# Performance work log

Measured on AMD Instinct MI355X. Metric: run time of the kernel, lower is better.

Reference implementation:

```python
import jax, jax.numpy as jnp
import numpy as np

N = 10000      # num nodes
E = 320000     # num edges
IN = 256       # in_dim
MP = 256       # mp_width
FL = 512       # fl_width
OUT = 64       # out_dim


def setup_inputs() -> dict:
    key = jax.random.key(0)
    ks = jax.random.split(key, 20)
    inp = {}
    inp["x"] = jax.random.normal(ks[0], (N, IN), dtype=jnp.float32)
    inp["edge_index"] = jax.random.randint(ks[1], (2, E), 0, N, dtype=jnp.int64)
    # iMP (frozen) linear layers: weight ~ N(0, 1) per nn.init.normal_(std=1.0)
    inp["mp_w0"] = jax.random.normal(ks[2], (IN, MP), dtype=jnp.float32)
    inp["mp_b0"] = jax.random.uniform(ks[3], (MP,), minval=-1.0, maxval=1.0) / np.sqrt(IN)
    inp["mp_w1"] = jax.random.normal(ks[4], (MP, MP), dtype=jnp.float32)
    inp["mp_b1"] = jax.random.uniform(ks[5], (MP,), minval=-1.0, maxval=1.0) / np.sqrt(MP)
    inp["mp_w2"] = jax.random.normal(ks[6], (MP, MP), dtype=jnp.float32)
    inp["mp_b2"] = jax.random.uniform(ks[7], (MP,), minval=-1.0, maxval=1.0) / np.sqrt(MP)
    # FC layers (torch default Linear init scale ~ 1/sqrt(fan_in))
    inp["fc_w0"] = jax.random.normal(ks[8], (MP, FL), dtype=jnp.float32) / np.sqrt(MP)
    inp["fc_b0"] = jnp.zeros((FL,), dtype=jnp.float32)
    inp["fc_w1"] = jax.random.normal(ks[9], (FL, FL), dtype=jnp.float32) / np.sqrt(FL)
    inp["fc_b1"] = jnp.zeros((FL,), dtype=jnp.float32)
    # injection projections
    inp["inj_w0"] = jax.random.normal(ks[10], (MP, FL), dtype=jnp.float32) / np.sqrt(MP)
    inp["inj_b0"] = jnp.zeros((FL,), dtype=jnp.float32)
    inp["inj_w1"] = jax.random.normal(ks[11], (MP, FL), dtype=jnp.float32) / np.sqrt(MP)
    inp["inj_b1"] = jnp.zeros((FL,), dtype=jnp.float32)
    inp["alpha"] = jnp.array(1.0, dtype=jnp.float32)
    inp["out_w"] = jax.random.normal(ks[12], (FL, OUT), dtype=jnp.float32) / np.sqrt(FL)
    inp["out_b"] = jnp.zeros((OUT,), dtype=jnp.float32)
    return inp


def _imp(x, w, b, row, col, deg_inv):
    # h = relu(W x); h /= deg; Ah = scatter_add over row of h[col]
    h = jax.nn.relu(x @ w + b) * deg_inv[:, None]      # [N, out]
    return jnp.zeros_like(h).at[row].add(h[col])       # gather + scatter-add


def reference(x, edge_index, mp_w0, mp_b0, mp_w1, mp_b1, mp_w2, mp_b2,
              fc_w0, fc_b0, fc_w1, fc_b1, inj_w0, inj_b0, inj_w1, inj_b1,
              alpha, out_w, out_b):
    row, col = edge_index[0], edge_index[1]
    deg = jax.ops.segment_sum(jnp.ones((E,), x.dtype), col, num_segments=N)
    # nodes with deg==0 never appear in col so clamping does not change output
    deg_inv = 1.0 / jnp.maximum(deg, 1.0)

    h = _imp(x, mp_w0, mp_b0, row, col, deg_inv)
    h = _imp(h, mp_w1, mp_b1, row, col, deg_inv)
    h = _imp(h, mp_w2, mp_b2, row, col, deg_inv)

    x_inject = h
    h = alpha * (jax.nn.relu(h) @ fc_w0 + fc_b0) + (x_inject @ inj_w0 + inj_b0)
    h = alpha * (jax.nn.relu(h) @ fc_w1 + fc_b1) + (x_inject @ inj_w1 + inj_b1)
    return h @ out_w + out_b
```

## Files before the change

### kernel.cpp

```cpp
#include <hip/hip_runtime.h>

#define N_NODES 10000
#define N_EDGES 320000
#define MPAD 10112
#define NBIN 10048
#define CAP 128
#define EBLKS 157
#define PREP_BLOCKS 768
#define PREP_TOT 656384L

typedef unsigned short u16;
typedef short bf16x8 __attribute__((ext_vector_type(8)));
typedef float f32x4 __attribute__((ext_vector_type(4)));

__device__ __forceinline__ u16 f2b(float f) {
  unsigned u = __builtin_bit_cast(unsigned, f);
  unsigned r = u + 0x7fffu + ((u >> 16) & 1u);
  return (u16)(r >> 16);
}
__device__ __forceinline__ unsigned pack2(float a, float b) {
  return (unsigned)f2b(a) | ((unsigned)f2b(b) << 16);
}
__device__ __forceinline__ float blo(unsigned u) { return __builtin_bit_cast(float, u << 16); }
__device__ __forceinline__ float bhi(unsigned u) { return __builtin_bit_cast(float, u & 0xffff0000u); }
__device__ __forceinline__ int4 cvt16(float4 a, float4 b) {
  int4 r;
  r.x = (int)pack2(a.x, a.y); r.y = (int)pack2(a.z, a.w);
  r.z = (int)pack2(b.x, b.y); r.w = (int)pack2(b.z, b.w);
  return r;
}

struct PP {
  const float *x; const int *ei;
  const float *w0, *w1, *w2, *fcw0, *injw0, *fcw1, *injw1, *outw;
  const float *fcb0, *injb0, *fcb1, *injb1, *alpha, *outb;
  u16 *w0t, *w1t, *w2t, *wc1t, *wft;
  float *bias1, *bf;
  int *cursor, *deg; u16 *csr;
};

__global__ __launch_bounds__(256) void prep_place(PP P) {
  const int tid = threadIdx.x, bid = blockIdx.x;

  if (bid < EBLKS) {
    const int e0 = bid * 2048;
#pragma unroll
    for (int j = 0; j < 2048; j += 256) {
      int e = e0 + j + tid;
      if (e < N_EDGES) {
        int r = P.ei[e];
        int c = P.ei[N_EDGES + e];
        atomicAdd(&P.deg[c], 1);
        int pos = atomicAdd(&P.cursor[r], 1);
        if (pos < CAP) P.csr[r * CAP + pos] = (u16)c;
      }
    }
    return;
  }

  const float alpha = P.alpha[0];
  const long stride = (long)PREP_BLOCKS * 256;
  for (long ii = (long)(bid - EBLKS) * 256 + tid; ii < PREP_TOT; ii += stride) {
    long i = ii;
    if (i < 196608) {
      int item = (int)(i >> 2), part = (int)i & 3;
      int n = item & 63, k = item >> 6;
      const float* fr = (k < 512) ? P.fcw1 + (size_t)k * 512
                                  : P.injw1 + (size_t)(k - 512) * 512;
      float a0 = 0.f, a1 = 0.f, a2 = 0.f, a3 = 0.f;
      const int j0 = part * 128;
#pragma unroll 4
      for (int j = j0; j < j0 + 128; j += 4) {
        float4 f = *(const float4*)(fr + j);
        a0 += f.x * P.outw[(j + 0) * 64 + n];
        a1 += f.y * P.outw[(j + 1) * 64 + n];
        a2 += f.z * P.outw[(j + 2) * 64 + n];
        a3 += f.w * P.outw[(j + 3) * 64 + n];
      }
      float acc = (a0 + a1) + (a2 + a3);
      acc += __shfl_xor(acc, 1, 64);
      acc += __shfl_xor(acc, 2, 64);
      if (part == 0) {
        if (k < 512) acc *= alpha;
        P.wft[n * 768 + k] = f2b(acc);
      }
      continue;
    }
    i -= 196608;
    if (i < 512) {
      int item = (int)(i >> 3), part = (int)i & 7;
      float acc = 0.f;
      const int j0 = part * 64;
#pragma unroll 4
      for (int j = j0; j < j0 + 64; ++j)
        acc += (alpha * P.fcb1[j] + P.injb1[j]) * P.outw[j * 64 + item];
      acc += __shfl_xor(acc, 1, 64);
      acc += __shfl_xor(acc, 2, 64);
      acc += __shfl_xor(acc, 4, 64);
      if (part == 0) P.bf[item] = P.outb[item] + acc;
      continue;
    }
    i -= 512;
    if (i < 65536) { P.w0t[i] = f2b(P.w0[(i & 255) * 256 + (i >> 8)]); continue; }
    i -= 65536;
    if (i < 65536) { P.w1t[i] = f2b(P.w1[(i & 255) * 256 + (i >> 8)]); continue; }
    i -= 65536;
    if (i < 65536) { P.w2t[i] = f2b(P.w2[(i & 255) * 256 + (i >> 8)]); continue; }
    i -= 65536;
    if (i < 262144) {
      int n = (int)(i >> 9), k = (int)(i & 511);
      float v = (k < 256) ? alpha * P.fcw0[k * 512 + n] : P.injw0[(k - 256) * 512 + n];
      P.wc1t[i] = f2b(v); continue;
    }
    i -= 262144;
    if (i < 512) { P.bias1[i] = alpha * P.fcb0[i] + P.injb0[i]; continue; }
  }
}

template<int K, bool RELU, bool SCALE, bool F32OUT, bool AF32>
__global__ __launch_bounds__(128) void gemm64(
    const void* __restrict__ Av, int lda,
    const u16* __restrict__ Bt,
    const float* __restrict__ bias,
    const int* __restrict__ deg,
    u16* __restrict__ Cb, float* __restrict__ Cf, int ldc)
{
  __shared__ u16 As[64 * 72];
  __shared__ u16 Bs[64 * 72];
  const int tid = threadIdx.x;
  const int m0 = blockIdx.x * 64;
  const int n0 = blockIdx.y * 64;
  const int wave = tid >> 6;
  const int lane = tid & 63;
  const int wr = wave * 32;
  const int lm = lane & 15;
  const int koff = (lane >> 4) * 8;

  const int srow = tid >> 2;
  const int scol = (tid & 3) * 16;
  const u16 *Ag0 = nullptr, *Ag1 = nullptr;
  const float *Af0 = nullptr, *Af1 = nullptr;
  if constexpr (AF32) {
    const int ar0 = min(m0 + srow, N_NODES - 1);
    const int ar1 = min(m0 + srow + 32, N_NODES - 1);
    Af0 = (const float*)Av + (size_t)ar0 * lda + scol;
    Af1 = (const float*)Av + (size_t)ar1 * lda + scol;
  } else {
    Ag0 = (const u16*)Av + (size_t)(m0 + srow) * lda + scol;
    Ag1 = (const u16*)Av + (size_t)(m0 + srow + 32) * lda + scol;
  }
  const u16* Bg0 = Bt + (size_t)(n0 + srow) * K + scol;
  const u16* Bg1 = Bt + (size_t)(n0 + srow + 32) * K + scol;
  u16* Asw0 = &As[srow * 72 + scol];
  u16* Asw1 = &As[(srow + 32) * 72 + scol];
  u16* Bsw0 = &Bs[srow * 72 + scol];
  u16* Bsw1 = &Bs[(srow + 32) * 72 + scol];

  f32x4 acc[2][4] = {};

  int4 pa0, pa1, pa2, pa3;
  if constexpr (AF32) {
    float4 f0 = *(const float4*)(Af0),     f1 = *(const float4*)(Af0 + 4);
    float4 f2 = *(const float4*)(Af0 + 8), f3 = *(const float4*)(Af0 + 12);
    float4 g0 = *(const float4*)(Af1),     g1 = *(const float4*)(Af1 + 4);
    float4 g2 = *(const float4*)(Af1 + 8), g3 = *(const float4*)(Af1 + 12);
    pa0 = cvt16(f0, f1); pa1 = cvt16(f2, f3);
    pa2 = cvt16(g0, g1); pa3 = cvt16(g2, g3);
  } else {
    pa0 = *(const int4*)(Ag0); pa1 = *(const int4*)(Ag0 + 8);
    pa2 = *(const int4*)(Ag1); pa3 = *(const int4*)(Ag1 + 8);
  }
  int4 pb0 = *(const int4*)(Bg0),     pb1 = *(const int4*)(Bg0 + 8);
  int4 pb2 = *(const int4*)(Bg1),     pb3 = *(const int4*)(Bg1 + 8);

#pragma unroll
  for (int kb = 0; kb < K; kb += 64) {
    __syncthreads();
    *(int4*)Asw0 = pa0; *(int4*)(Asw0 + 8) = pa1;
    *(int4*)Asw1 = pa2; *(int4*)(Asw1 + 8) = pa3;
    *(int4*)Bsw0 = pb0; *(int4*)(Bsw0 + 8) = pb1;
    *(int4*)Bsw1 = pb2; *(int4*)(Bsw1 + 8) = pb3;
    __syncthreads();
    if (kb + 64 < K) {
      if constexpr (AF32) {
        const float* a0 = Af0 + kb + 64;
        const float* a1 = Af1 + kb + 64;
        float4 f0 = *(const float4*)(a0),     f1 = *(const float4*)(a0 + 4);
        float4 f2 = *(const float4*)(a0 + 8), f3 = *(const float4*)(a0 + 12);
        float4 g0 = *(const float4*)(a1),     g1 = *(const float4*)(a1 + 4);
        float4 g2 = *(const float4*)(a1 + 8), g3 = *(const float4*)(a1 + 12);
        pa0 = cvt16(f0, f1); pa1 = cvt16(f2, f3);
        pa2 = cvt16(g0, g1); pa3 = cvt16(g2, g3);
      } else {
        pa0 = *(const int4*)(Ag0 + kb + 64); pa1 = *(const int4*)(Ag0 + kb + 72);
        pa2 = *(const int4*)(Ag1 + kb + 64); pa3 = *(const int4*)(Ag1 + kb + 72);
      }
      pb0 = *(const int4*)(Bg0 + kb + 64); pb1 = *(const int4*)(Bg0 + kb + 72);
      pb2 = *(const int4*)(Bg1 + kb + 64); pb3 = *(const int4*)(Bg1 + kb + 72);
    }
#pragma unroll
    for (int ks = 0; ks < 2; ++ks) {
      bf16x8 af[2], bf[4];
#pragma unroll
      for (int mi = 0; mi < 2; ++mi)
        af[mi] = *(const bf16x8*)&As[(wr + mi * 16 + lm) * 72 + ks * 32 + koff];
#pragma unroll
      for (int ni = 0; ni < 4; ++ni)
        bf[ni] = *(const bf16x8*)&Bs[(ni * 16 + lm) * 72 + ks * 32 + koff];
#pragma unroll
      for (int mi = 0; mi < 2; ++mi)
#pragma unroll
        for (int ni = 0; ni < 4; ++ni)
          acc[mi][ni] = __builtin_amdgcn_mfma_f32_16x16x32_bf16(af[mi], bf[ni], acc[mi][ni], 0, 0, 0);
    }
  }

  const int q4 = (lane >> 4) * 4;
#pragma unroll
  for (int mi = 0; mi < 2; ++mi) {
#pragma unroll
    for (int ni = 0; ni < 4; ++ni) {
      const int gc = n0 + ni * 16 + lm;
      const float bv = bias[gc];
#pragma unroll
      for (int r = 0; r < 4; ++r) {
        const int gr = m0 + wr + mi * 16 + q4 + r;
        float v = acc[mi][ni][r] + bv;
        if (RELU) v = fmaxf(v, 0.f);
        if (SCALE) v *= 1.0f / fmaxf((float)deg[gr], 1.0f);
        if (F32OUT) {
          if (gr < N_NODES) Cf[(size_t)gr * ldc + gc] = v;
        } else {
          Cb[(size_t)gr * ldc + gc] = f2b(v);
        }
      }
    }
  }
}

__global__ __launch_bounds__(128) void gemm_fold(
    const u16* __restrict__ Ar,
    const u16* __restrict__ Ah,
    const u16* __restrict__ Bt,
    const float* __restrict__ bias,
    float* __restrict__ Cf)
{
  const int K = 768;
  __shared__ u16 As[64 * 72];
  __shared__ u16 Bs[64 * 72];
  const int tid = threadIdx.x;
  const int m0 = blockIdx.x * 64;
  const int n0 = 0;
  const int wave = tid >> 6;
  const int lane = tid & 63;
  const int wr = wave * 32;
  const int lm = lane & 15;
  const int koff = (lane >> 4) * 8;

  const int srow = tid >> 2;
  const int scol = (tid & 3) * 16;
  const int ar0 = m0 + srow, ar1 = m0 + srow + 32;
  auto aptr = [&](int row, int col) -> const u16* {
    return (col < 512) ? Ar + (size_t)row * 512 + col
                       : Ah + (size_t)row * 512 + (col - 512);
  };
  const u16* Bg0 = Bt + (size_t)(n0 + srow) * K + scol;
  const u16* Bg1 = Bt + (size_t)(n0 + srow + 32) * K + scol;
  u16* Asw0 = &As[srow * 72 + scol];
  u16* Asw1 = &As[(srow + 32) * 72 + scol];
  u16* Bsw0 = &Bs[srow * 72 + scol];
  u16* Bsw1 = &Bs[(srow + 32) * 72 + scol];

  f32x4 acc[2][4] = {};

  int4 pa0 = *(const int4*)aptr(ar0, scol);
  int4 pa1 = *(const int4*)aptr(ar0, scol + 8);
  int4 pa2 = *(const int4*)aptr(ar1, scol);
  int4 pa3 = *(const int4*)aptr(ar1, scol + 8);
  int4 pb0 = *(const int4*)(Bg0), pb1 = *(const int4*)(Bg0 + 8);
  int4 pb2 = *(const int4*)(Bg1), pb3 = *(const int4*)(Bg1 + 8);

#pragma unroll
  for (int kb = 0; kb < K; kb += 64) {
    __syncthreads();
    *(int4*)Asw0 = pa0; *(int4*)(Asw0 + 8) = pa1;
    *(int4*)Asw1 = pa2; *(int4*)(Asw1 + 8) = pa3;
    *(int4*)Bsw0 = pb0; *(int4*)(Bsw0 + 8) = pb1;
    *(int4*)Bsw1 = pb2; *(int4*)(Bsw1 + 8) = pb3;
    __syncthreads();
    if (kb + 64 < K) {
      int c = kb + 64 + scol;
      pa0 = *(const int4*)aptr(ar0, c);
      pa1 = *(const int4*)aptr(ar0, c + 8);
      pa2 = *(const int4*)aptr(ar1, c);
      pa3 = *(const int4*)aptr(ar1, c + 8);
      pb0 = *(const int4*)(Bg0 + kb + 64); pb1 = *(const int4*)(Bg0 + kb + 72);
      pb2 = *(const int4*)(Bg1 + kb + 64); pb3 = *(const int4*)(Bg1 + kb + 72);
    }
#pragma unroll
    for (int ks = 0; ks < 2; ++ks) {
      bf16x8 af[2], bf[4];
#pragma unroll
      for (int mi = 0; mi < 2; ++mi)
        af[mi] = *(const bf16x8*)&As[(wr + mi * 16 + lm) * 72 + ks * 32 + koff];
#pragma unroll
      for (int ni = 0; ni < 4; ++ni)
        bf[ni] = *(const bf16x8*)&Bs[(ni * 16 + lm) * 72 + ks * 32 + koff];
#pragma unroll
      for (int mi = 0; mi < 2; ++mi)
#pragma unroll
        for (int ni = 0; ni < 4; ++ni)
          acc[mi][ni] = __builtin_amdgcn_mfma_f32_16x16x32_bf16(af[mi], bf[ni], acc[mi][ni], 0, 0, 0);
    }
  }

  const int q4 = (lane >> 4) * 4;
#pragma unroll
  for (int mi = 0; mi < 2; ++mi) {
#pragma unroll
    for (int ni = 0; ni < 4; ++ni) {
      const int gc = ni * 16 + lm;
      const float bv = bias[gc];
#pragma unroll
      for (int r = 0; r < 4; ++r) {
        const int gr = m0 + wr + mi * 16 + q4 + r;
        if (gr < N_NODES) Cf[(size_t)gr * 64 + gc] = acc[mi][ni][r] + bv;
      }
    }
  }
}

__global__ __launch_bounds__(256) void aggregate(
    const u16* __restrict__ tmp, const int* __restrict__ cnt,
    const u16* __restrict__ csr, u16* __restrict__ out0,
    u16* __restrict__ A1, int mode)
{
  const int wv = threadIdx.x >> 6;
  const int lane = threadIdx.x & 63;
  const int r = blockIdx.x * 4 + wv;
  const int half = lane >> 5;
  const int q = lane & 31;
  int n = cnt[r]; if (n > CAP) n = CAP;
  const int beg = r * CAP, end = beg + n;
  const size_t feat = (size_t)q * 16;
  const char* tb = (const char*)tmp;

  float s0 = 0.f, s1 = 0.f, s2 = 0.f, s3 = 0.f, s4 = 0.f, s5 = 0.f, s6 = 0.f, s7 = 0.f;
  int i = beg;
  for (; i + 8 <= end; i += 8) {
    uint4 v[4];
#pragma unroll
    for (int j = 0; j < 4; ++j)
      v[j] = *(const uint4*)(tb + (size_t)csr[i + 2 * j + half] * 512 + feat);
#pragma unroll
    for (int j = 0; j < 4; ++j) {
      s0 += blo(v[j].x); s1 += bhi(v[j].x); s2 += blo(v[j].y); s3 += bhi(v[j].y);
      s4 += blo(v[j].z); s5 += bhi(v[j].z); s6 += blo(v[j].w); s7 += bhi(v[j].w);
    }
  }
  for (; i < end; i += 2) {
    int id = i + half;
    if (id < end) {
      uint4 v = *(const uint4*)(tb + (size_t)csr[id] * 512 + feat);
      s0 += blo(v.x); s1 += bhi(v.x); s2 += blo(v.y); s3 += bhi(v.y);
      s4 += blo(v.z); s5 += bhi(v.z); s6 += blo(v.w); s7 += bhi(v.w);
    }
  }
  const int src = lane ^ 32;
  s0 += __shfl(s0, src, 64); s1 += __shfl(s1, src, 64);
  s2 += __shfl(s2, src, 64); s3 += __shfl(s3, src, 64);
  s4 += __shfl(s4, src, 64); s5 += __shfl(s5, src, 64);
  s6 += __shfl(s6, src, 64); s7 += __shfl(s7, src, 64);

  if (half == 0) {
    uint4 pv;
    pv.x = pack2(s0, s1); pv.y = pack2(s2, s3);
    pv.z = pack2(s4, s5); pv.w = pack2(s6, s7);
    if (mode == 0) {
      *(uint4*)((char*)out0 + (size_t)r * 512 + feat) = pv;
    } else {
      uint4 pr;
      pr.x = pack2(fmaxf(s0, 0.f), fmaxf(s1, 0.f));
      pr.y = pack2(fmaxf(s2, 0.f), fmaxf(s3, 0.f));
      pr.z = pack2(fmaxf(s4, 0.f), fmaxf(s5, 0.f));
      pr.w = pack2(fmaxf(s6, 0.f), fmaxf(s7, 0.f));
      *(uint4*)((char*)A1 + (size_t)r * 1024 + feat) = pr;
      *(uint4*)((char*)A1 + (size_t)r * 1024 + 512 + feat) = pv;
    }
  }
}

extern "C" void kernel_launch(void* const* d_in, const int* in_sizes, int n_in,
                              void* d_out, int out_size, void* d_ws, size_t ws_size,
                              hipStream_t stream) {
  const int* ei = (const int*)d_in[1];

  char* p = (char*)d_ws;
  auto carve = [&](size_t bytes) -> void* {
    void* r = (void*)p;
    p += (bytes + 255) & ~(size_t)255;
    return r;
  };
  int*   deg     = (int*)carve(MPAD * 4);
  int*   cursor  = (int*)carve(NBIN * 4);
  u16*   csr     = (u16*)carve((size_t)NBIN * CAP * 2);
  float* bias1   = (float*)carve(512 * 4);
  float* bf      = (float*)carve(64 * 4);
  u16* w0t   = (u16*)carve(65536 * 2);
  u16* w1t   = (u16*)carve(65536 * 2);
  u16* w2t   = (u16*)carve(65536 * 2);
  u16* wc1t  = (u16*)carve(262144 * 2);
  u16* wft   = (u16*)carve(49152 * 2);
  u16* tmp   = (u16*)carve((size_t)MPAD * 256 * 2);
  u16* h     = (u16*)carve((size_t)MPAD * 256 * 2);
  u16* cat1  = (u16*)carve((size_t)MPAD * 512 * 2);
  u16* relu1 = (u16*)carve((size_t)MPAD * 512 * 2);

  PP pp;
  pp.x = (const float*)d_in[0];
  pp.ei = ei;
  pp.w0 = (const float*)d_in[2];
  pp.w1 = (const float*)d_in[4];
  pp.w2 = (const float*)d_in[6];
  pp.fcw0 = (const float*)d_in[8];
  pp.fcw1 = (const float*)d_in[10];
  pp.injw0 = (const float*)d_in[12];
  pp.injw1 = (const float*)d_in[14];
  pp.outw = (const float*)d_in[17];
  pp.fcb0 = (const float*)d_in[9];
  pp.injb0 = (const float*)d_in[13];
  pp.fcb1 = (const float*)d_in[11];
  pp.injb1 = (const float*)d_in[15];
  pp.alpha = (const float*)d_in[16];
  pp.outb = (const float*)d_in[18];
  pp.w0t = w0t; pp.w1t = w1t; pp.w2t = w2t;
  pp.wc1t = wc1t; pp.wft = wft;
  pp.bias1 = bias1; pp.bf = bf;
  pp.cursor = cursor; pp.deg = deg; pp.csr = csr;

  const float* mp_b0 = (const float*)d_in[3];
  const float* mp_b1 = (const float*)d_in[5];
  const float* mp_b2 = (const float*)d_in[7];
  float* out = (float*)d_out;

  hipMemsetAsync(deg, 0, (size_t)(MPAD + NBIN) * 4, stream);
  prep_place<<<EBLKS + PREP_BLOCKS, 256, 0, stream>>>(pp);

  dim3 gmp(MPAD / 64, 4), gfc(MPAD / 64, 8), go(MPAD / 64, 1);
  gemm64<256, true, true, false, true ><<<gmp, 128, 0, stream>>>(pp.x, 256, w0t, mp_b0, deg, tmp, nullptr, 256);
  aggregate<<<2500, 256, 0, stream>>>(tmp, cursor, csr, h, nullptr, 0);
  gemm64<256, true, true, false, false><<<gmp, 128, 0, stream>>>(h, 256, w1t, mp_b1, deg, tmp, nullptr, 256);
  aggregate<<<2500, 256, 0, stream>>>(tmp, cursor, csr, h, nullptr, 0);
  gemm64<256, true, true, false, false><<<gmp, 128, 0, stream>>>(h, 256, w2t, mp_b2, deg, tmp, nullptr, 256);
  aggregate<<<2500, 256, 0, stream>>>(tmp, cursor, csr, nullptr, cat1, 1);
  gemm64<512, true, false, false, false><<<gfc, 128, 0, stream>>>(cat1, 512, wc1t, bias1, nullptr, relu1, nullptr, 512);
  gemm_fold<<<go, 128, 0, stream>>>(relu1, cat1 + 256, wft, bf, out);
}
```

Baseline: 245.3 us.

## Fuse first MP GEMM into prep kernel and split aggregation into feature halves

```diff
diff --git a/kernel.cpp b/kernel.cpp
--- a/kernel.cpp
+++ b/kernel.cpp
@@ -5,9 +5,13 @@
 #define MPAD 10112
 #define NBIN 10048
 #define CAP 128
-#define EBLKS 157
-#define PREP_BLOCKS 768
-#define PREP_TOT 656384L
+
+#define E1BLKS 313
+#define G1BLKS 632
+#define WB0    (E1BLKS + G1BLKS)
+#define WBLKS  1536
+#define GRID1  (WB0 + WBLKS)
+#define WPREP_TOT 590848L
 
 typedef unsigned short u16;
 typedef short bf16x8 __attribute__((ext_vector_type(8)));
@@ -29,60 +33,144 @@
   r.z = (int)pack2(b.x, b.y); r.w = (int)pack2(b.z, b.w);
   return r;
 }
+__device__ __forceinline__ void ldA(const float* a, int4& lo, int4& hi) {
+  float4 f0 = *(const float4*)(a),     f1 = *(const float4*)(a + 4);
+  float4 f2 = *(const float4*)(a + 8), f3 = *(const float4*)(a + 12);
+  lo = cvt16(f0, f1); hi = cvt16(f2, f3);
+}
+__device__ __forceinline__ void ldB(const float* w, int n, int k0, int4& lo, int4& hi) {
+  const float* p = w + (size_t)k0 * 256 + n;
+  lo.x = (int)pack2(p[0],    p[256]);  lo.y = (int)pack2(p[512],  p[768]);
+  lo.z = (int)pack2(p[1024], p[1280]); lo.w = (int)pack2(p[1536], p[1792]);
+  hi.x = (int)pack2(p[2048], p[2304]); hi.y = (int)pack2(p[2560], p[2816]);
+  hi.z = (int)pack2(p[3072], p[3328]); hi.w = (int)pack2(p[3584], p[3840]);
+}
 
 struct PP {
   const float *x; const int *ei;
   const float *w0, *w1, *w2, *fcw0, *injw0, *fcw1, *injw1, *outw;
-  const float *fcb0, *injb0, *fcb1, *injb1, *alpha, *outb;
-  u16 *w0t, *w1t, *w2t, *wc1t, *wft;
+  const float *fcb0, *injb0, *fcb1, *injb1, *alpha, *outb, *b0;
+  u16 *w1t, *w2t, *wc1t, *wft, *tmp;
   float *bias1, *bf;
   int *cursor, *deg; u16 *csr;
 };
 
-__global__ __launch_bounds__(256) void prep_place(PP P) {
+__global__ __launch_bounds__(128, 4) void fused1(PP F) {
   const int tid = threadIdx.x, bid = blockIdx.x;
-
-  if (bid < EBLKS) {
-    const int e0 = bid * 2048;
-#pragma unroll
-    for (int j = 0; j < 2048; j += 256) {
+  __shared__ u16 As[64 * 72];
+  __shared__ u16 Bs[64 * 72];
+
+  if (bid < E1BLKS) {
+    const int e0 = bid * 1024;
+#pragma unroll
+    for (int j = 0; j < 1024; j += 128) {
       int e = e0 + j + tid;
       if (e < N_EDGES) {
-        int r = P.ei[e];
-        int c = P.ei[N_EDGES + e];
-        atomicAdd(&P.deg[c], 1);
-        int pos = atomicAdd(&P.cursor[r], 1);
-        if (pos < CAP) P.csr[r * CAP + pos] = (u16)c;
+        int r = F.ei[e];
+        int c = F.ei[N_EDGES + e];
+        atomicAdd(&F.deg[c], 1);
+        int pos = atomicAdd(&F.cursor[r], 1);
+        if (pos < CAP) F.csr[r * CAP + pos] = (u16)c;
       }
     }
     return;
   }
 
-  const float alpha = P.alpha[0];
-  const long stride = (long)PREP_BLOCKS * 256;
-  for (long ii = (long)(bid - EBLKS) * 256 + tid; ii < PREP_TOT; ii += stride) {
+  if (bid < WB0) {
+    const int gb = bid - E1BLKS;
+    const int m0 = (gb >> 2) * 64;
+    const int n0 = (gb & 3) * 64;
+    const int wave = tid >> 6, lane = tid & 63;
+    const int wr = wave * 32, lm = lane & 15, koff = (lane >> 4) * 8;
+    const int srow = tid >> 2, scol = (tid & 3) * 16;
+
+    const int ar0 = min(m0 + srow, N_NODES - 1);
+    const int ar1 = min(m0 + srow + 32, N_NODES - 1);
+    const float* Af0 = F.x + (size_t)ar0 * 256 + scol;
+    const float* Af1 = F.x + (size_t)ar1 * 256 + scol;
+    const int bn0 = n0 + srow, bn1 = n0 + srow + 32;
+    u16* Asw0 = &As[srow * 72 + scol];
+    u16* Asw1 = &As[(srow + 32) * 72 + scol];
+    u16* Bsw0 = &Bs[srow * 72 + scol];
+    u16* Bsw1 = &Bs[(srow + 32) * 72 + scol];
+
+    f32x4 acc[2][4] = {};
+    int4 pa0, pa1, pa2, pa3, pb0, pb1, pb2, pb3;
+    ldA(Af0, pa0, pa1); ldA(Af1, pa2, pa3);
+    ldB(F.w0, bn0, scol, pb0, pb1); ldB(F.w0, bn1, scol, pb2, pb3);
+
+#pragma unroll
+    for (int kb = 0; kb < 256; kb += 64) {
+      __syncthreads();
+      *(int4*)Asw0 = pa0; *(int4*)(Asw0 + 8) = pa1;
+      *(int4*)Asw1 = pa2; *(int4*)(Asw1 + 8) = pa3;
+      *(int4*)Bsw0 = pb0; *(int4*)(Bsw0 + 8) = pb1;
+      *(int4*)Bsw1 = pb2; *(int4*)(Bsw1 + 8) = pb3;
+      __syncthreads();
+      if (kb + 64 < 256) {
+        ldA(Af0 + kb + 64, pa0, pa1); ldA(Af1 + kb + 64, pa2, pa3);
+        ldB(F.w0, bn0, kb + 64 + scol, pb0, pb1);
+        ldB(F.w0, bn1, kb + 64 + scol, pb2, pb3);
+      }
+#pragma unroll
+      for (int ks = 0; ks < 2; ++ks) {
+        bf16x8 af[2], bfr[4];
+#pragma unroll
+        for (int mi = 0; mi < 2; ++mi)
+          af[mi] = *(const bf16x8*)&As[(wr + mi * 16 + lm) * 72 + ks * 32 + koff];
+#pragma unroll
+        for (int ni = 0; ni < 4; ++ni)
+          bfr[ni] = *(const bf16x8*)&Bs[(ni * 16 + lm) * 72 + ks * 32 + koff];
+#pragma unroll
+        for (int mi = 0; mi < 2; ++mi)
+#pragma unroll
+          for (int ni = 0; ni < 4; ++ni)
+            acc[mi][ni] = __builtin_amdgcn_mfma_f32_16x16x32_bf16(af[mi], bfr[ni], acc[mi][ni], 0, 0, 0);
+      }
+    }
+
+    const int q4 = (lane >> 4) * 4;
+#pragma unroll
+    for (int mi = 0; mi < 2; ++mi) {
+#pragma unroll
+      for (int ni = 0; ni < 4; ++ni) {
+        const int gc = n0 + ni * 16 + lm;
+        const float bv = F.b0[gc];
+#pragma unroll
+        for (int r = 0; r < 4; ++r) {
+          const int gr = m0 + wr + mi * 16 + q4 + r;
+          F.tmp[(size_t)gr * 256 + gc] = f2b(fmaxf(acc[mi][ni][r] + bv, 0.f));
+        }
+      }
+    }
+    return;
+  }
+
+  const float alpha = F.alpha[0];
+  const long stride = (long)WBLKS * 128;
+  for (long ii = (long)(bid - WB0) * 128 + tid; ii < WPREP_TOT; ii += stride) {
     long i = ii;
     if (i < 196608) {
       int item = (int)(i >> 2), part = (int)i & 3;
       int n = item & 63, k = item >> 6;
-      const float* fr = (k < 512) ? P.fcw1 + (size_t)k * 512
-                                  : P.injw1 + (size_t)(k - 512) * 512;
+      const float* fr = (k < 512) ? F.fcw1 + (size_t)k * 512
+                                  : F.injw1 + (size_t)(k - 512) * 512;
       float a0 = 0.f, a1 = 0.f, a2 = 0.f, a3 = 0.f;
       const int j0 = part * 128;
 #pragma unroll 4
       for (int j = j0; j < j0 + 128; j += 4) {
         float4 f = *(const float4*)(fr + j);
-        a0 += f.x * P.outw[(j + 0) * 64 + n];
-        a1 += f.y * P.outw[(j + 1) * 64 + n];
-        a2 += f.z * P.outw[(j + 2) * 64 + n];
-        a3 += f.w * P.outw[(j + 3) * 64 + n];
+        a0 += f.x * F.outw[(j + 0) * 64 + n];
+        a1 += f.y * F.outw[(j + 1) * 64 + n];
+        a2 += f.z * F.outw[(j + 2) * 64 + n];
+        a3 += f.w * F.outw[(j + 3) * 64 + n];
       }
       float acc = (a0 + a1) + (a2 + a3);
       acc += __shfl_xor(acc, 1, 64);
       acc += __shfl_xor(acc, 2, 64);
       if (part == 0) {
         if (k < 512) acc *= alpha;
-        P.wft[n * 768 + k] = f2b(acc);
+        F.wft[n * 768 + k] = f2b(acc);
       }
       continue;
     }
@@ -93,33 +181,31 @@
       const int j0 = part * 64;
 #pragma unroll 4
       for (int j = j0; j < j0 + 64; ++j)
-        acc += (alpha * P.fcb1[j] + P.injb1[j]) * P.outw[j * 64 + item];
+        acc += (alpha * F.fcb1[j] + F.injb1[j]) * F.outw[j * 64 + item];
       acc += __shfl_xor(acc, 1, 64);
       acc += __shfl_xor(acc, 2, 64);
       acc += __shfl_xor(acc, 4, 64);
-      if (part == 0) P.bf[item] = P.outb[item] + acc;
+      if (part == 0) F.bf[item] = F.outb[item] + acc;
       continue;
     }
     i -= 512;
-    if (i < 65536) { P.w0t[i] = f2b(P.w0[(i & 255) * 256 + (i >> 8)]); continue; }
+    if (i < 65536) { F.w1t[i] = f2b(F.w1[(i & 255) * 256 + (i >> 8)]); continue; }
     i -= 65536;
-    if (i < 65536) { P.w1t[i] = f2b(P.w1[(i & 255) * 256 + (i >> 8)]); continue; }
-    i -= 65536;
-    if (i < 65536) { P.w2t[i] = f2b(P.w2[(i & 255) * 256 + (i >> 8)]); continue; }
+    if (i < 65536) { F.w2t[i] = f2b(F.w2[(i & 255) * 256 + (i >> 8)]); continue; }
     i -= 65536;
     if (i < 262144) {
       int n = (int)(i >> 9), k = (int)(i & 511);
-      float v = (k < 256) ? alpha * P.fcw0[k * 512 + n] : P.injw0[(k - 256) * 512 + n];
-      P.wc1t[i] = f2b(v); continue;
+      float v = (k < 256) ? alpha * F.fcw0[k * 512 + n] : F.injw0[(k - 256) * 512 + n];
+      F.wc1t[i] = f2b(v); continue;
     }
     i -= 262144;
-    if (i < 512) { P.bias1[i] = alpha * P.fcb0[i] + P.injb0[i]; continue; }
-  }
-}
-
-template<int K, bool RELU, bool SCALE, bool F32OUT, bool AF32>
+    if (i < 512) { F.bias1[i] = alpha * F.fcb0[i] + F.injb0[i]; continue; }
+  }
+}
+
+template<int K, bool RELU, bool SCALE, bool F32OUT>
 __global__ __launch_bounds__(128) void gemm64(
-    const void* __restrict__ Av, int lda,
+    const u16* __restrict__ A, int lda,
     const u16* __restrict__ Bt,
     const float* __restrict__ bias,
     const int* __restrict__ deg,
@@ -138,17 +224,8 @@
 
   const int srow = tid >> 2;
   const int scol = (tid & 3) * 16;
-  const u16 *Ag0 = nullptr, *Ag1 = nullptr;
-  const float *Af0 = nullptr, *Af1 = nullptr;
-  if constexpr (AF32) {
-    const int ar0 = min(m0 + srow, N_NODES - 1);
-    const int ar1 = min(m0 + srow + 32, N_NODES - 1);
-    Af0 = (const float*)Av + (size_t)ar0 * lda + scol;
-    Af1 = (const float*)Av + (size_t)ar1 * lda + scol;
-  } else {
-    Ag0 = (const u16*)Av + (size_t)(m0 + srow) * lda + scol;
-    Ag1 = (const u16*)Av + (size_t)(m0 + srow + 32) * lda + scol;
-  }
+  const u16* Ag0 = A + (size_t)(m0 + srow) * lda + scol;
+  const u16* Ag1 = A + (size_t)(m0 + srow + 32) * lda + scol;
   const u16* Bg0 = Bt + (size_t)(n0 + srow) * K + scol;
   const u16* Bg1 = Bt + (size_t)(n0 + srow + 32) * K + scol;
   u16* Asw0 = &As[srow * 72 + scol];
@@ -158,18 +235,8 @@
 
   f32x4 acc[2][4] = {};
 
-  int4 pa0, pa1, pa2, pa3;
-  if constexpr (AF32) {
-    float4 f0 = *(const float4*)(Af0),     f1 = *(const float4*)(Af0 + 4);
-    float4 f2 = *(const float4*)(Af0 + 8), f3 = *(const float4*)(Af0 + 12);
-    float4 g0 = *(const float4*)(Af1),     g1 = *(const float4*)(Af1 + 4);
-    float4 g2 = *(const float4*)(Af1 + 8), g3 = *(const float4*)(Af1 + 12);
-    pa0 = cvt16(f0, f1); pa1 = cvt16(f2, f3);
-    pa2 = cvt16(g0, g1); pa3 = cvt16(g2, g3);
-  } else {
-    pa0 = *(const int4*)(Ag0); pa1 = *(const int4*)(Ag0 + 8);
-    pa2 = *(const int4*)(Ag1); pa3 = *(const int4*)(Ag1 + 8);
-  }
+  int4 pa0 = *(const int4*)(Ag0),     pa1 = *(const int4*)(Ag0 + 8);
+  int4 pa2 = *(const int4*)(Ag1),     pa3 = *(const int4*)(Ag1 + 8);
   int4 pb0 = *(const int4*)(Bg0),     pb1 = *(const int4*)(Bg0 + 8);
   int4 pb2 = *(const int4*)(Bg1),     pb3 = *(const int4*)(Bg1 + 8);
 
@@ -182,19 +249,8 @@
     *(int4*)Bsw1 = pb2; *(int4*)(Bsw1 + 8) = pb3;
     __syncthreads();
     if (kb + 64 < K) {
-      if constexpr (AF32) {
-        const float* a0 = Af0 + kb + 64;
-        const float* a1 = Af1 + kb + 64;
-        float4 f0 = *(const float4*)(a0),     f1 = *(const float4*)(a0 + 4);
-        float4 f2 = *(const float4*)(a0 + 8), f3 = *(const float4*)(a0 + 12);
-        float4 g0 = *(const float4*)(a1),     g1 = *(const float4*)(a1 + 4);
-        float4 g2 = *(const float4*)(a1 + 8), g3 = *(const float4*)(a1 + 12);
-        pa0 = cvt16(f0, f1); pa1 = cvt16(f2, f3);
-        pa2 = cvt16(g0, g1); pa3 = cvt16(g2, g3);
-      } else {
-        pa0 = *(const int4*)(Ag0 + kb + 64); pa1 = *(const int4*)(Ag0 + kb + 72);
-        pa2 = *(const int4*)(Ag1 + kb + 64); pa3 = *(const int4*)(Ag1 + kb + 72);
-      }
+      pa0 = *(const int4*)(Ag0 + kb + 64); pa1 = *(const int4*)(Ag0 + kb + 72);
+      pa2 = *(const int4*)(Ag1 + kb + 64); pa3 = *(const int4*)(Ag1 + kb + 72);
       pb0 = *(const int4*)(Bg0 + kb + 64); pb1 = *(const int4*)(Bg0 + kb + 72);
       pb2 = *(const int4*)(Bg1 + kb + 64); pb3 = *(const int4*)(Bg1 + kb + 72);
     }
@@ -330,10 +386,11 @@
   }
 }
 
+template<bool DSC>
 __global__ __launch_bounds__(256) void aggregate(
     const u16* __restrict__ tmp, const int* __restrict__ cnt,
-    const u16* __restrict__ csr, u16* __restrict__ out0,
-    u16* __restrict__ A1, int mode)
+    const u16* __restrict__ csr, const int* __restrict__ deg,
+    u16* __restrict__ out0, u16* __restrict__ A1, int mode, int fh)
 {
   const int wv = threadIdx.x >> 6;
   const int lane = threadIdx.x & 63;
@@ -342,50 +399,55 @@
   const int q = lane & 31;
   int n = cnt[r]; if (n > CAP) n = CAP;
   const int beg = r * CAP, end = beg + n;
-  const size_t feat = (size_t)q * 16;
+  const size_t feat = (size_t)fh * 256 + (size_t)q * 8;
   const char* tb = (const char*)tmp;
 
-  float s0 = 0.f, s1 = 0.f, s2 = 0.f, s3 = 0.f, s4 = 0.f, s5 = 0.f, s6 = 0.f, s7 = 0.f;
+  float s0 = 0.f, s1 = 0.f, s2 = 0.f, s3 = 0.f;
   int i = beg;
   for (; i + 8 <= end; i += 8) {
-    uint4 v[4];
-#pragma unroll
-    for (int j = 0; j < 4; ++j)
-      v[j] = *(const uint4*)(tb + (size_t)csr[i + 2 * j + half] * 512 + feat);
+    uint2 v[4]; float sc[4];
 #pragma unroll
     for (int j = 0; j < 4; ++j) {
-      s0 += blo(v[j].x); s1 += bhi(v[j].x); s2 += blo(v[j].y); s3 += bhi(v[j].y);
-      s4 += blo(v[j].z); s5 += bhi(v[j].z); s6 += blo(v[j].w); s7 += bhi(v[j].w);
+      int c = csr[i + 2 * j + half];
+      v[j] = *(const uint2*)(tb + (size_t)c * 512 + feat);
+      sc[j] = DSC ? 1.0f / fmaxf((float)deg[c], 1.0f) : 1.0f;
+    }
+#pragma unroll
+    for (int j = 0; j < 4; ++j) {
+      if (DSC) {
+        s0 += sc[j] * blo(v[j].x); s1 += sc[j] * bhi(v[j].x);
+        s2 += sc[j] * blo(v[j].y); s3 += sc[j] * bhi(v[j].y);
+      } else {
+        s0 += blo(v[j].x); s1 += bhi(v[j].x);
+        s2 += blo(v[j].y); s3 += bhi(v[j].y);
+      }
     }
   }
   for (; i < end; i += 2) {
     int id = i + half;
     if (id < end) {
-      uint4 v = *(const uint4*)(tb + (size_t)csr[id] * 512 + feat);
-      s0 += blo(v.x); s1 += bhi(v.x); s2 += blo(v.y); s3 += bhi(v.y);
-      s4 += blo(v.z); s5 += bhi(v.z); s6 += blo(v.w); s7 += bhi(v.w);
+      int c = csr[id];
+      uint2 v = *(const uint2*)(tb + (size_t)c * 512 + feat);
+      float sc = DSC ? 1.0f / fmaxf((float)deg[c], 1.0f) : 1.0f;
+      s0 += sc * blo(v.x); s1 += sc * bhi(v.x);
+      s2 += sc * blo(v.y); s3 += sc * bhi(v.y);
     }
   }
   const int src = lane ^ 32;
   s0 += __shfl(s0, src, 64); s1 += __shfl(s1, src, 64);
   s2 += __shfl(s2, src, 64); s3 += __shfl(s3, src, 64);
-  s4 += __shfl(s4, src, 64); s5 += __shfl(s5, src, 64);
-  s6 += __shfl(s6, src, 64); s7 += __shfl(s7, src, 64);
 
   if (half == 0) {
-    uint4 pv;
+    uint2 pv;
     pv.x = pack2(s0, s1); pv.y = pack2(s2, s3);
-    pv.z = pack2(s4, s5); pv.w = pack2(s6, s7);
     if (mode == 0) {
-      *(uint4*)((char*)out0 + (size_t)r * 512 + feat) = pv;
+      *(uint2*)((char*)out0 + (size_t)r * 512 + feat) = pv;
     } else {
-      uint4 pr;
+      uint2 pr;
       pr.x = pack2(fmaxf(s0, 0.f), fmaxf(s1, 0.f));
       pr.y = pack2(fmaxf(s2, 0.f), fmaxf(s3, 0.f));
-      pr.z = pack2(fmaxf(s4, 0.f), fmaxf(s5, 0.f));
-      pr.w = pack2(fmaxf(s6, 0.f), fmaxf(s7, 0.f));
-      *(uint4*)((char*)A1 + (size_t)r * 1024 + feat) = pr;
-      *(uint4*)((char*)A1 + (size_t)r * 1024 + 512 + feat) = pv;
+      *(uint2*)((char*)A1 + (size_t)r * 1024 + feat) = pr;
+      *(uint2*)((char*)A1 + (size_t)r * 1024 + 512 + feat) = pv;
     }
   }
 }
@@ -406,7 +468,6 @@
   u16*   csr     = (u16*)carve((size_t)NBIN * CAP * 2);
   float* bias1   = (float*)carve(512 * 4);
   float* bf      = (float*)carve(64 * 4);
-  u16* w0t   = (u16*)carve(65536 * 2);
   u16* w1t   = (u16*)carve(65536 * 2);
   u16* w2t   = (u16*)carve(65536 * 2);
   u16* wc1t  = (u16*)carve(262144 * 2);
@@ -433,26 +494,28 @@
   pp.injb1 = (const float*)d_in[15];
   pp.alpha = (const float*)d_in[16];
   pp.outb = (const float*)d_in[18];
-  pp.w0t = w0t; pp.w1t = w1t; pp.w2t = w2t;
-  pp.wc1t = wc1t; pp.wft = wft;
+  pp.b0 = (const float*)d_in[3];
+  pp.w1t = w1t; pp.w2t = w2t;
+  pp.wc1t = wc1t; pp.wft = wft; pp.tmp = tmp;
   pp.bias1 = bias1; pp.bf = bf;
   pp.cursor = cursor; pp.deg = deg; pp.csr = csr;
 
-  const float* mp_b0 = (const float*)d_in[3];
   const float* mp_b1 = (const float*)d_in[5];
   const float* mp_b2 = (const float*)d_in[7];
   float* out = (float*)d_out;
 
   hipMemsetAsync(deg, 0, (size_t)(MPAD + NBIN) * 4, stream);
-  prep_place<<<EBLKS + PREP_BLOCKS, 256, 0, stream>>>(pp);
+  fused1<<<GRID1, 128, 0, stream>>>(pp);
 
   dim3 gmp(MPAD / 64, 4), gfc(MPAD / 64, 8), go(MPAD / 64, 1);
-  gemm64<256, true, true, false, true ><<<gmp, 128, 0, stream>>>(pp.x, 256, w0t, mp_b0, deg, tmp, nullptr, 256);
-  aggregate<<<2500, 256, 0, stream>>>(tmp, cursor, csr, h, nullptr, 0);
-  gemm64<256, true, true, false, false><<<gmp, 128, 0, stream>>>(h, 256, w1t, mp_b1, deg, tmp, nullptr, 256);
-  aggregate<<<2500, 256, 0, stream>>>(tmp, cursor, csr, h, nullptr, 0);
-  gemm64<256, true, true, false, false><<<gmp, 128, 0, stream>>>(h, 256, w2t, mp_b2, deg, tmp, nullptr, 256);
-  aggregate<<<2500, 256, 0, stream>>>(tmp, cursor, csr, nullptr, cat1, 1);
-  gemm64<512, true, false, false, false><<<gfc, 128, 0, stream>>>(cat1, 512, wc1t, bias1, nullptr, relu1, nullptr, 512);
+  aggregate<true ><<<2500, 256, 0, stream>>>(tmp, cursor, csr, deg, h, nullptr, 0, 0);
+  aggregate<true ><<<2500, 256, 0, stream>>>(tmp, cursor, csr, deg, h, nullptr, 0, 1);
+  gemm64<256, true, true, false><<<gmp, 128, 0, stream>>>(h, 256, w1t, mp_b1, deg, tmp, nullptr, 256);
+  aggregate<false><<<2500, 256, 0, stream>>>(tmp, cursor, csr, nullptr, h, nullptr, 0, 0);
+  aggregate<false><<<2500, 256, 0, stream>>>(tmp, cursor, csr, nullptr, h, nullptr, 0, 1);
+  gemm64<256, true, true, false><<<gmp, 128, 0, stream>>>(h, 256, w2t, mp_b2, deg, tmp, nullptr, 256);
+  aggregate<false><<<2500, 256, 0, stream>>>(tmp, cursor, csr, nullptr, nullptr, cat1, 1, 0);
+  aggregate<false><<<2500, 256, 0, stream>>>(tmp, cursor, csr, nullptr, nullptr, cat1, 1, 1);
+  gemm64<512, true, false, false><<<gfc, 128, 0, stream>>>(cat1, 512, wc1t, bias1, nullptr, relu1, nullptr, 512);
   gemm_fold<<<go, 128, 0, stream>>>(relu1, cat1 + 256, wft, bf, out);
 }
```

After: 265.1 us. 1.08x slower.
